# Performance work log

Measured on AMD Instinct MI355X. Metric: run time of the kernel, lower is better.

## Reference

```python
import jax, jax.numpy as jnp
import numpy as np

HIDDEN = 768
HEADS = 12
HEAD_DIM = HIDDEN // HEADS  # 64


def setup_inputs() -> dict:
    key = jax.random.key(0)
    ks = jax.random.split(key, 7)
    B, S = 4, 2048
    std = 0.02
    return {
        "hidden_states": jax.random.normal(ks[0], (B, S, HIDDEN), dtype=jnp.float32),
        "attention_mask": jnp.zeros((B, 1, 1, S), dtype=jnp.float32),
        "Wq": jax.random.normal(ks[1], (HIDDEN, HIDDEN), dtype=jnp.float32) * std,
        "bq": jnp.zeros((HIDDEN,), dtype=jnp.float32),
        "Wk": jax.random.normal(ks[2], (HIDDEN, HIDDEN), dtype=jnp.float32) * std,
        "bk": jnp.zeros((HIDDEN,), dtype=jnp.float32),
        "Wv": jax.random.normal(ks[3], (HIDDEN, HIDDEN), dtype=jnp.float32) * std,
        "bv": jnp.zeros((HIDDEN,), dtype=jnp.float32),
    }


def _split_heads(x):
    # [B, S, HIDDEN] -> [B, H, S, D]
    B, S, _ = x.shape
    return x.reshape(B, S, HEADS, HEAD_DIM).transpose(0, 2, 1, 3)


def reference(hidden_states, attention_mask, Wq, bq, Wk, bk, Wv, bv):
    q = _split_heads(hidden_states @ Wq + bq)
    k = _split_heads(hidden_states @ Wk + bk)
    v = _split_heads(hidden_states @ Wv + bv)
    # [B, H, S, S] full score matrix (as in the original non-fused impl)
    scores = jnp.einsum("bhqd,bhkd->bhqk", q, k) / jnp.sqrt(
        jnp.asarray(HEAD_DIM, dtype=q.dtype)
    )
    scores = scores + attention_mask
    probs = jax.nn.softmax(scores, axis=-1)
    # dropout prob = 0.0 -> identity in eval
    ctx = jnp.einsum("bhqk,bhkd->bhqd", probs, v)
    B, H, S, D = ctx.shape
    return ctx.transpose(0, 2, 1, 3).reshape(B, S, H * D)
```

## Files before the change

kernel.cpp:

```cpp
#include <hip/hip_runtime.h>

typedef __bf16 bf16;
typedef __attribute__((ext_vector_type(8))) __bf16 bf16x8;
typedef __attribute__((ext_vector_type(4))) __bf16 bf16x4;
typedef __attribute__((ext_vector_type(4))) float f32x4;
typedef __attribute__((ext_vector_type(16))) float f32x16;
typedef __attribute__((ext_vector_type(4))) unsigned int u32x4;

#define DI __device__ __forceinline__

static constexpr int HID = 768;
static constexpr int SEQ = 2048;
static constexpr int NH  = 12;
static constexpr int HD  = 64;

DI void gload16(const void* g, void* l) {
  __builtin_amdgcn_global_load_lds(
      (const __attribute__((address_space(1))) void*)g,
      (__attribute__((address_space(3))) void*)l, 16, 0, 0);
}
DI int swz128(int row, int cb) { return row * 128 + (cb ^ ((row & 7) << 4)); }

DI unsigned cvtpk_bf16(float lo, float hi) {
  unsigned d;
  asm("v_cvt_pk_bf16_f32 %0, %1, %2" : "=v"(d) : "v"(lo), "v"(hi));
  return d;
}
DI void permswap(unsigned &a, unsigned &b) {
  asm("v_permlane32_swap_b32 %0, %1" : "+v"(a), "+v"(b));
}

__global__ void k_convert_x(const float* __restrict__ X, bf16* __restrict__ Xb, int n8) {
  int i = blockIdx.x * blockDim.x + threadIdx.x;
  if (i >= n8) return;
  const f32x4* Xv = (const f32x4*)X;
  f32x4 a = Xv[2 * i], b = Xv[2 * i + 1];
  bf16x8 o;
  o[0] = (bf16)a[0]; o[1] = (bf16)a[1]; o[2] = (bf16)a[2]; o[3] = (bf16)a[3];
  o[4] = (bf16)b[0]; o[5] = (bf16)b[1]; o[6] = (bf16)b[2]; o[7] = (bf16)b[3];
  *(bf16x8*)(Xb + (size_t)i * 8) = o;
}

__global__ void k_transpose_w(const float* __restrict__ Wq, const float* __restrict__ Wk,
                              const float* __restrict__ Wv, bf16* __restrict__ WT) {
  int z = blockIdx.z;
  const float* W = (z == 0) ? Wq : (z == 1) ? Wk : Wv;
  bf16* WTz = WT + (size_t)z * HID * HID;
  int k0 = blockIdx.x * 64, n0 = blockIdx.y * 64;
  __shared__ float t[64][65];
  int tt = threadIdx.x;
  for (int p = 0; p < 4; ++p) {
    int r = p * 16 + (tt >> 4), c4 = (tt & 15) * 4;
    f32x4 v = *(const f32x4*)(W + (size_t)(k0 + r) * HID + n0 + c4);
    t[c4 + 0][r] = v[0]; t[c4 + 1][r] = v[1]; t[c4 + 2][r] = v[2]; t[c4 + 3][r] = v[3];
  }
  __syncthreads();
  for (int p = 0; p < 4; ++p) {
    int rn = p * 16 + (tt >> 4), c4 = (tt & 15) * 4;
    bf16x4 o;
    o[0] = (bf16)t[rn][c4]; o[1] = (bf16)t[rn][c4 + 1];
    o[2] = (bf16)t[rn][c4 + 2]; o[3] = (bf16)t[rn][c4 + 3];
    *(bf16x4*)(WTz + (size_t)(n0 + rn) * HID + k0 + c4) = o;
  }
}

__global__ __launch_bounds__(256, 2)
void k_qkv_gemm(const bf16* __restrict__ Xb, const bf16* __restrict__ WT,
                const float* __restrict__ bq, const float* __restrict__ bk,
                const float* __restrict__ bv,
                bf16* __restrict__ Qb, bf16* __restrict__ Kb, bf16* __restrict__ VTb) {
  int z = blockIdx.z;
  const bf16* WTz = WT + (size_t)z * HID * HID;
  const float* bias = (z == 0) ? bq : (z == 1) ? bk : bv;

  int m0 = blockIdx.x * 128, n0 = blockIdx.y * 128;
  __shared__ char lds[32768];
  int w = threadIdx.x >> 6, l = threadIdx.x & 63;
  int wr = w >> 1, wc = w & 1;

  f32x4 acc[4][4] = {};

  for (int it = 0; it < HID / 64; ++it) {
    int k0 = it * 64;
    __syncthreads();
    for (int j = 0; j < 8; ++j) {
      int base = w * 8192 + j * 1024;
      int o = base + l * 16;
      const char* src;
      if (o < 16384) {
        int row = o >> 7;
        int cb = (o & 127) ^ ((row & 7) << 4);
        src = (const char*)(Xb + (size_t)(m0 + row) * HID + k0) + cb;
      } else {
        int o2 = o - 16384;
        int row = o2 >> 7;
        int cb = (o2 & 127) ^ ((row & 7) << 4);
        src = (const char*)(WTz + (size_t)(n0 + row) * HID + k0) + cb;
      }
      gload16(src, lds + base);
    }
    __syncthreads();

    for (int kk = 0; kk < 2; ++kk) {
      bf16x8 af[4], bfr[4];
      int cb = kk * 64 + ((l >> 4) << 4);
      for (int ms = 0; ms < 4; ++ms) {
        int row = wr * 64 + ms * 16 + (l & 15);
        af[ms] = *(const bf16x8*)(lds + swz128(row, cb));
      }
      for (int ns = 0; ns < 4; ++ns) {
        int row = wc * 64 + ns * 16 + (l & 15);
        bfr[ns] = *(const bf16x8*)(lds + 16384 + swz128(row, cb));
      }
      for (int ms = 0; ms < 4; ++ms)
        for (int ns = 0; ns < 4; ++ns)
          acc[ms][ns] = __builtin_amdgcn_mfma_f32_16x16x32_bf16(af[ms], bfr[ns], acc[ms][ns], 0, 0, 0);
    }
  }

  if (z == 2) {
    #pragma unroll
    for (int ns = 0; ns < 4; ++ns) {
      int col = n0 + wc * 64 + ns * 16 + (l & 15);
      float bvv = bias[col];
      int h = col >> 6, d = col & 63;
      #pragma unroll
      for (int ms = 0; ms < 4; ++ms) {
        int m = m0 + wr * 64 + ms * 16 + ((l >> 4) << 2);
        int bb = m >> 11, s = m & 2047;
        bf16x4 pk;
        #pragma unroll
        for (int r = 0; r < 4; ++r) pk[r] = (bf16)(acc[ms][ns][r] + bvv);
        size_t base = (size_t)(bb * NH + h) * HD * SEQ;
        size_t idx = base + (size_t)(s >> 6) * 4096 + (size_t)((s >> 3) & 7) * 512
                     + (size_t)d * 8 + (s & 7);
        *(bf16x4*)(VTb + idx) = pk;
      }
    }
  } else if (z == 1) {
    for (int ns = 0; ns < 4; ++ns) {
      int col = n0 + wc * 64 + ns * 16 + (l & 15);
      float bvv = bias[col];
      int h = col >> 6, d = col & 63;
      for (int ms = 0; ms < 4; ++ms) {
        for (int r = 0; r < 4; ++r) {
          int m = m0 + wr * 64 + ms * 16 + ((l >> 4) << 2) + r;
          int bb = m >> 11, s = m & 2047;
          float v = acc[ms][ns][r] + bvv;
          size_t base = (size_t)(bb * NH + h) * SEQ * HD;
          size_t idx = base + (size_t)(s >> 6) * 4096 + (size_t)(d >> 3) * 512
                       + (size_t)(s & 63) * 8 + (d & 7);
          Kb[idx] = (bf16)v;
        }
      }
    }
  } else {
    for (int ns = 0; ns < 4; ++ns) {
      int col = n0 + wc * 64 + ns * 16 + (l & 15);
      float bvv = bias[col];
      int h = col >> 6, d = col & 63;
      for (int ms = 0; ms < 4; ++ms) {
        for (int r = 0; r < 4; ++r) {
          int m = m0 + wr * 64 + ms * 16 + ((l >> 4) << 2) + r;
          int bb = m >> 11, s = m & 2047;
          float v = (acc[ms][ns][r] + bvv) * 0.125f;
          Qb[(((size_t)(bb * NH + h) * SEQ + s) << 6) + d] = (bf16)v;
        }
      }
    }
  }
}

__global__ __launch_bounds__(256, 3)
void k_attn(const bf16* __restrict__ Qb, const bf16* __restrict__ Kb,
            const bf16* __restrict__ VTb, const float* __restrict__ mask,
            float* __restrict__ out) {
  __shared__ char lds[33280];
  constexpr int NT = SEQ / 64;
  int bh = blockIdx.x;
  int b = bh / NH, h = bh % NH;
  int q0 = blockIdx.y * 128;
  int w = threadIdx.x >> 6, l = threadIdx.x & 63;
  int q = l & 31, hi = l >> 5;
  const bf16* Qp = Qb + (size_t)bh * SEQ * HD;
  const char* Kbase = (const char*)(Kb + (size_t)bh * SEQ * HD);
  const char* VTbase = (const char*)(VTb + (size_t)bh * HD * SEQ);
  const float* mb = mask + (size_t)b * SEQ;

  bf16x8 qf[4];
  #pragma unroll
  for (int dstep = 0; dstep < 4; ++dstep)
    qf[dstep] = *(const bf16x8*)(Qp + (size_t)(q0 + w * 32 + q) * HD + dstep * 16 + hi * 8);

  f32x16 acc[2] = {};
  float psum = 0.f;

  int rbase = hi * 1024 + q * 16;

  auto stage = [&](int c, int kt) {
    size_t t = (size_t)kt * 8192;
    int off = w * 2048;
    #pragma unroll
    for (int j = 0; j < 2; ++j)
      gload16(Kbase + t + off + j * 1024 + l * 16,
              lds + c * 16384 + off + j * 1024);
    #pragma unroll
    for (int j = 0; j < 2; ++j)
      gload16(VTbase + t + off + j * 1024 + l * 16,
              lds + c * 16384 + 8192 + off + j * 1024);
  };

  stage(0, 0);
  __syncthreads();

  int cur = 0;
  for (int kt = 0; kt < NT; ++kt) {
    if (kt + 1 < NT) stage(cur ^ 1, kt + 1);

    f32x4 mm[2][4];
    #pragma unroll
    for (int kh = 0; kh < 2; ++kh)
      #pragma unroll
      for (int blk = 0; blk < 4; ++blk)
        mm[kh][blk] = *(const f32x4*)(mb + kt * 64 + kh * 32 + blk * 8 + hi * 4);

    const char* Kl = lds + cur * 16384 + rbase;
    const char* Vl = lds + cur * 16384 + 8192 + rbase;

    #pragma unroll
    for (int kh = 0; kh < 2; ++kh) {
      bf16x8 kfh[4], vfk[4];
      #pragma unroll
      for (int dstep = 0; dstep < 4; ++dstep)
        kfh[dstep] = *(const bf16x8*)(Kl + dstep * 2048 + kh * 512);
      #pragma unroll
      for (int half = 0; half < 2; ++half)
        #pragma unroll
        for (int db = 0; db < 2; ++db)
          vfk[half * 2 + db] =
              *(const bf16x8*)(Vl + (kh * 2 + half) * 2048 + db * 512);

      f32x16 p;
      #pragma unroll
      for (int r = 0; r < 16; ++r) p[r] = mm[kh][r >> 2][r & 3];
      __builtin_amdgcn_s_setprio(1);
      #pragma unroll
      for (int dstep = 0; dstep < 4; ++dstep)
        p = __builtin_amdgcn_mfma_f32_32x32x16_bf16(kfh[dstep], qf[dstep], p, 0, 0, 0);
      __builtin_amdgcn_s_setprio(0);

      #pragma unroll
      for (int r = 0; r < 16; ++r) {
        float e = __expf(p[r]);
        p[r] = e;
        psum += e;
      }

      #pragma unroll
      for (int half = 0; half < 2; ++half) {
        int base = half * 8;
        unsigned a0 = cvtpk_bf16(p[base + 0], p[base + 1]);
        unsigned a1 = cvtpk_bf16(p[base + 2], p[base + 3]);
        unsigned a2 = cvtpk_bf16(p[base + 4], p[base + 5]);
        unsigned a3 = cvtpk_bf16(p[base + 6], p[base + 7]);
        permswap(a0, a2);
        permswap(a1, a3);
        u32x4 pk; pk[0] = a0; pk[1] = a1; pk[2] = a2; pk[3] = a3;
        bf16x8 PA = __builtin_bit_cast(bf16x8, pk);
        __builtin_amdgcn_s_setprio(1);
        #pragma unroll
        for (int db = 0; db < 2; ++db)
          acc[db] = __builtin_amdgcn_mfma_f32_32x32x16_bf16(PA, vfk[half * 2 + db], acc[db], 0, 0, 0);
        __builtin_amdgcn_s_setprio(0);
      }
    }

    __syncthreads();
    cur ^= 1;
  }

  float tot = psum + __shfl_xor(psum, 32);
  float* lsumL = (float*)(lds + 32768 + w * 128);
  if (l < 32) lsumL[l] = tot;
  __syncthreads();
  f32x4 lv[4];
  #pragma unroll
  for (int blk = 0; blk < 4; ++blk)
    lv[blk] = *(const f32x4*)(lsumL + blk * 8 + hi * 4);
  float inv[16];
  #pragma unroll
  for (int r = 0; r < 16; ++r) inv[r] = 1.0f / lv[r >> 2][r & 3];

  #pragma unroll
  for (int db = 0; db < 2; ++db)
    #pragma unroll
    for (int r = 0; r < 16; ++r) {
      int s = q0 + w * 32 + (r & 3) + 8 * (r >> 2) + 4 * hi;
      out[((size_t)(b * SEQ + s)) * HID + h * HD + db * 32 + q] = acc[db][r] * inv[r];
    }
}

extern "C" void kernel_launch(void* const* d_in, const int* in_sizes, int n_in,
                              void* d_out, int out_size, void* d_ws, size_t ws_size,
                              hipStream_t stream) {
  const float* X    = (const float*)d_in[0];
  const float* mask = (const float*)d_in[1];
  const float* Wq   = (const float*)d_in[2];
  const float* bq   = (const float*)d_in[3];
  const float* Wk   = (const float*)d_in[4];
  const float* bk   = (const float*)d_in[5];
  const float* Wv   = (const float*)d_in[6];
  const float* bv   = (const float*)d_in[7];
  float* out = (float*)d_out;
  char* ws = (char*)d_ws;

  const size_t SZ_XB = (size_t)8192 * HID * 2;
  const size_t SZ_WT = (size_t)3 * HID * HID * 2;
  const size_t SZ_M  = (size_t)4 * NH * SEQ * HD * 2;
  bf16* Xb  = (bf16*)(ws);
  bf16* WT  = (bf16*)(ws + SZ_XB);
  bf16* Qb  = (bf16*)(ws + SZ_XB + SZ_WT);
  bf16* Kb  = (bf16*)(ws + SZ_XB + SZ_WT + SZ_M);
  bf16* VTb = (bf16*)(ws + SZ_XB + SZ_WT + 2 * SZ_M);

  k_convert_x<<<3072, 256, 0, stream>>>(X, Xb, 8192 * HID / 8);
  k_transpose_w<<<dim3(12, 12, 3), 256, 0, stream>>>(Wq, Wk, Wv, WT);
  k_qkv_gemm<<<dim3(64, 6, 3), 256, 0, stream>>>(Xb, WT, bq, bk, bv, Qb, Kb, VTb);
  k_attn<<<dim3(48, 16), 256, 0, stream>>>(Qb, Kb, VTb, mask, out);
}
```

Before: 120.6 us.

## Triple-buffer K/V tiles in attention kernel with prefetch distance two

The attention loop moves from double to triple buffering of K and V^T tiles in LDS. Loads for tile kt+2 are issued while tile kt is computed, and partial vmcnt waits replace full __syncthreads so that one tile's loads can stay in flight across the barrier. LDS use grows to about 49.6 KB per block, which may cut the occupancy of 3 blocks per CU set in launch bounds. The mask loads are also counted in vmcnt, so the wait count of 4 depends on how the compiler orders those loads.

Measured after the change: 119.7 us. No clear change (-0.7%).

```diff
diff --git a/kernel.cpp b/kernel.cpp
--- a/kernel.cpp
+++ b/kernel.cpp
@@ -175,7 +175,7 @@
 void k_attn(const bf16* __restrict__ Qb, const bf16* __restrict__ Kb,
             const bf16* __restrict__ VTb, const float* __restrict__ mask,
             float* __restrict__ out) {
-  __shared__ char lds[33280];
+  __shared__ char lds[49664];
   constexpr int NT = SEQ / 64;
   int bh = blockIdx.x;
   int b = bh / NH, h = bh % NH;
@@ -197,35 +197,40 @@
 
   int rbase = hi * 1024 + q * 16;
 
-  auto stage = [&](int c, int kt) {
+  auto stage = [&](char* buf, int kt) {
     size_t t = (size_t)kt * 8192;
     int off = w * 2048;
     #pragma unroll
     for (int j = 0; j < 2; ++j)
-      gload16(Kbase + t + off + j * 1024 + l * 16,
-              lds + c * 16384 + off + j * 1024);
+      gload16(Kbase + t + off + j * 1024 + l * 16, buf + off + j * 1024);
     #pragma unroll
     for (int j = 0; j < 2; ++j)
-      gload16(VTbase + t + off + j * 1024 + l * 16,
-              lds + c * 16384 + 8192 + off + j * 1024);
+      gload16(VTbase + t + off + j * 1024 + l * 16, buf + 8192 + off + j * 1024);
   };
 
-  stage(0, 0);
-  __syncthreads();
-
-  int cur = 0;
+  char* bufA = lds;
+  char* bufB = lds + 16384;
+  char* bufC = lds + 32768;
+
+  stage(bufA, 0);
+  stage(bufB, 1);
+  asm volatile("s_waitcnt vmcnt(4)" ::: "memory");
+  __builtin_amdgcn_s_barrier();
+  __builtin_amdgcn_sched_barrier(0);
+
   for (int kt = 0; kt < NT; ++kt) {
-    if (kt + 1 < NT) stage(cur ^ 1, kt + 1);
-
     f32x4 mm[2][4];
     #pragma unroll
     for (int kh = 0; kh < 2; ++kh)
       #pragma unroll
       for (int blk = 0; blk < 4; ++blk)
         mm[kh][blk] = *(const f32x4*)(mb + kt * 64 + kh * 32 + blk * 8 + hi * 4);
-
-    const char* Kl = lds + cur * 16384 + rbase;
-    const char* Vl = lds + cur * 16384 + 8192 + rbase;
+    __builtin_amdgcn_sched_barrier(0);
+
+    if (kt + 2 < NT) stage(bufC, kt + 2);
+
+    const char* Kl = bufA + rbase;
+    const char* Vl = bufA + 8192 + rbase;
 
     #pragma unroll
     for (int kh = 0; kh < 2; ++kh) {
@@ -275,12 +280,21 @@
       }
     }
 
-    __syncthreads();
-    cur ^= 1;
+    if (kt < NT - 1) {
+      if (kt + 2 < NT) {
+        asm volatile("s_waitcnt vmcnt(4)" ::: "memory");
+      } else {
+        asm volatile("s_waitcnt vmcnt(0)" ::: "memory");
+      }
+      __builtin_amdgcn_s_barrier();
+      __builtin_amdgcn_sched_barrier(0);
+    }
+
+    char* tmp = bufA; bufA = bufB; bufB = bufC; bufC = tmp;
   }
 
   float tot = psum + __shfl_xor(psum, 32);
-  float* lsumL = (float*)(lds + 32768 + w * 128);
+  float* lsumL = (float*)(lds + 49152 + w * 128);
   if (l < 32) lsumL[l] = tot;
   __syncthreads();
   f32x4 lv[4];
```
